# Performance work log

Hardware: AMD Instinct MI355X
Metric: run time of the kernel (lower is better)

Reference implementation:

```python
import jax, jax.numpy as jnp
import numpy as np

N_ENT = 50000
N_EDGE = 500000
D = 256          # ent_hidden_size
H1, C1 = 8, 64   # conv1: heads=8, out=64, concat -> 512
NEG_SLOPE = 0.2
LN_EPS = 1e-5


def setup_inputs() -> dict:
    key = jax.random.key(0)
    ks = jax.random.split(key, 12)
    s = 0.05  # small init scale for numerical sanity
    return {
        "edge_index": jax.random.randint(ks[0], (2, N_EDGE), 0, N_ENT),
        "x": jax.random.normal(ks[1], (N_ENT, D), dtype=jnp.float32),
        "ln_w": jnp.ones((D,), jnp.float32),
        "ln_b": jnp.zeros((D,), jnp.float32),
        "W1": jax.random.normal(ks[2], (D, H1 * C1), dtype=jnp.float32) * s,
        "att_src1": jax.random.normal(ks[3], (H1, C1), dtype=jnp.float32) * s,
        "att_dst1": jax.random.normal(ks[4], (H1, C1), dtype=jnp.float32) * s,
        "b1": jnp.zeros((H1 * C1,), jnp.float32),
        "W2": jax.random.normal(ks[5], (H1 * C1, D), dtype=jnp.float32) * s,
        "att_src2": jax.random.normal(ks[6], (1, D), dtype=jnp.float32) * s,
        "att_dst2": jax.random.normal(ks[7], (1, D), dtype=jnp.float32) * s,
        "b2": jnp.zeros((D,), jnp.float32),
    }


def _gat_conv(x, edge_index, W, att_src, att_dst, bias, heads, out_ch, concat):
    """PyG GATConv (shared src/dst lin, add_self_loops=True, eval-mode dropout)."""
    n = x.shape[0]
    loops = jnp.arange(n)
    src = jnp.concatenate([edge_index[0], loops])  # [E+N]
    dst = jnp.concatenate([edge_index[1], loops])

    h = (x @ W).reshape(n, heads, out_ch)                 # [N,H,C]
    a_src = jnp.sum(h * att_src[None], axis=-1)           # [N,H]
    a_dst = jnp.sum(h * att_dst[None], axis=-1)           # [N,H]

    e = jax.nn.leaky_relu(a_src[src] + a_dst[dst], NEG_SLOPE)  # [E+N,H]
    # per-destination segment softmax (every dst has a self-loop -> no empties)
    m = jax.lax.stop_gradient(jax.ops.segment_max(e, dst, num_segments=n))
    p = jnp.exp(e - m[dst])
    denom = jax.ops.segment_sum(p, dst, num_segments=n)
    alpha = p / denom[dst]                                # [E+N,H]

    out = jax.ops.segment_sum(h[src] * alpha[..., None], dst, num_segments=n)  # [N,H,C]
    out = out.reshape(n, heads * out_ch) if concat else out.mean(axis=1)
    return out + bias


def reference(edge_index, x, ln_w, ln_b, W1, att_src1, att_dst1, b1,
              W2, att_src2, att_dst2, b2):
    # LayerNorm(ent_hidden), eps=1e-5; dropouts are eval-mode no-ops
    mu = jnp.mean(x, axis=-1, keepdims=True)
    var = jnp.var(x, axis=-1, keepdims=True)
    h = (x - mu) / jnp.sqrt(var + LN_EPS) * ln_w + ln_b
    h = jax.nn.elu(_gat_conv(h, edge_index, W1, att_src1, att_dst1, b1, H1, C1, True))
    return _gat_conv(h, edge_index, W2, att_src2, att_dst2, b2, 1, D, False)
```

## Files before the change

### kernel.cpp

```cpp
#include <hip/hip_runtime.h>
#include <hip/hip_bf16.h>
#include <cstdint>

#define N_ENT  50000
#define N_EDGE 500000
#define D_IN   256
constexpr int ETOT = N_EDGE + N_ENT;

typedef __attribute__((ext_vector_type(8))) short bfrag;
typedef __attribute__((ext_vector_type(4))) float f4acc;
typedef __attribute__((ext_vector_type(4))) float f32x4;
typedef __attribute__((ext_vector_type(8))) short s16x8;

__device__ __forceinline__ float lrelu(float x) { return x > 0.f ? x : 0.2f * x; }
__device__ __forceinline__ float eluf(float x)  { return x > 0.f ? x : (expf(x) - 1.f); }
__device__ __forceinline__ short to_bf16(float f) {
    __hip_bfloat16 b = __float2bfloat16(f);
    return *(short*)&b;
}
__device__ __forceinline__ float2 bf2_to_f32(unsigned int u) {
    float2 r;
    r.x = __uint_as_float(u << 16);
    r.y = __uint_as_float(u & 0xffff0000u);
    return r;
}

__global__ __launch_bounds__(256) void prep_kernel(const float* __restrict__ x,
        const float* __restrict__ lnw, const float* __restrict__ lnb,
        short* __restrict__ y, const int* __restrict__ ei, int* __restrict__ cnt,
        const float* __restrict__ W1, short* __restrict__ W1T,
        const float* __restrict__ W2, short* __restrict__ W2T)
{
    int blk = blockIdx.x;
    if (blk < 12500) {
        int n = blk * 4 + (threadIdx.x >> 6);
        int lane = threadIdx.x & 63;
        const f32x4 v = __builtin_nontemporal_load((const f32x4*)(x + (size_t)n * D_IN + lane * 4));
        float s  = v.x + v.y + v.z + v.w;
        float sq = v.x*v.x + v.y*v.y + v.z*v.z + v.w*v.w;
        #pragma unroll
        for (int off = 1; off < 64; off <<= 1) {
            s  += __shfl_xor(s, off);
            sq += __shfl_xor(sq, off);
        }
        float mean = s * (1.f / 256.f);
        float var  = sq * (1.f / 256.f) - mean * mean;
        float rstd = rsqrtf(var + 1e-5f);
        float4 wv = *(const float4*)(lnw + lane * 4);
        float4 bv = *(const float4*)(lnb + lane * 4);
        short4 o;
        o.x = to_bf16((v.x - mean) * rstd * wv.x + bv.x);
        o.y = to_bf16((v.y - mean) * rstd * wv.y + bv.y);
        o.z = to_bf16((v.z - mean) * rstd * wv.z + bv.z);
        o.w = to_bf16((v.w - mean) * rstd * wv.w + bv.w);
        *(short4*)(y + (size_t)n * D_IN + lane * 4) = o;
    } else if (blk < 14454) {
        int e = (blk - 12500) * 256 + threadIdx.x;
        if (e < N_EDGE) atomicAdd(&cnt[ei[N_EDGE + e]], 1);
    } else if (blk < 14966) {
        int i = (blk - 14454) * 256 + threadIdx.x;
        int r = i >> 9, c = i & 511;
        W1T[c * 256 + r] = to_bf16(W1[i]);
    } else {
        int i = (blk - 14966) * 256 + threadIdx.x;
        int r = i >> 8, c = i & 255;
        W2T[c * 512 + r] = to_bf16(W2[i]);
    }
}

template<int NN, int KK, bool FUSE_DOTS>
__global__ __launch_bounds__(256) void gemm_mfma(const short* __restrict__ A,
        const short* __restrict__ BT, short* __restrict__ C,
        const float* __restrict__ att_s, const float* __restrict__ att_d,
        float* __restrict__ a_s, float* __restrict__ a_d, int M)
{
    __shared__ short As[128 * 32];
    __shared__ short Bs[128 * 32];
    const int tid  = threadIdx.x;
    const int w    = tid >> 6;
    const int l    = tid & 63;
    const int wm   = w >> 1, wn = w & 1;
    const int m0   = blockIdx.y * 128;
    const int n0   = blockIdx.x * 128;
    const int quad = l >> 4;
    const int ln16 = l & 15;
    const int rl   = l >> 2;
    const int cs   = l & 3;

    f4acc acc[4][4];
    #pragma unroll
    for (int i = 0; i < 4; ++i)
        #pragma unroll
        for (int j = 0; j < 4; ++j)
            acc[i][j] = (f4acc){0.f, 0.f, 0.f, 0.f};

    for (int k0 = 0; k0 < KK; k0 += 32) {
        __syncthreads();
        #pragma unroll
        for (int tt = 0; tt < 2; ++tt) {
            int t   = w * 2 + tt;
            int row = t * 16 + rl;
            int ca  = cs ^ ((row >> 1) & 3);
            const short* ga = A + (size_t)(m0 + row) * KK + k0 + ca * 8;
            __builtin_amdgcn_global_load_lds(
                (const __attribute__((address_space(1))) unsigned int*)ga,
                (__attribute__((address_space(3))) unsigned int*)&As[t * 512], 16, 0, 0);
            const short* gb = BT + (size_t)(n0 + row) * KK + k0 + ca * 8;
            __builtin_amdgcn_global_load_lds(
                (const __attribute__((address_space(1))) unsigned int*)gb,
                (__attribute__((address_space(3))) unsigned int*)&Bs[t * 512], 16, 0, 0);
        }
        __syncthreads();
        bfrag af[4], bf[4];
        #pragma unroll
        for (int i = 0; i < 4; ++i) {
            int r = wm * 64 + i * 16 + ln16;
            af[i] = *(const bfrag*)&As[r * 32 + (quad ^ ((r >> 1) & 3)) * 8];
            int rn = wn * 64 + i * 16 + ln16;
            bf[i] = *(const bfrag*)&Bs[rn * 32 + (quad ^ ((rn >> 1) & 3)) * 8];
        }
        #pragma unroll
        for (int i = 0; i < 4; ++i)
            #pragma unroll
            for (int j = 0; j < 4; ++j)
                acc[i][j] = __builtin_amdgcn_mfma_f32_16x16x32_bf16(af[i], bf[j], acc[i][j], 0, 0, 0);
    }

    float as_c[4], ad_c[4];
    if constexpr (FUSE_DOTS) {
        #pragma unroll
        for (int j = 0; j < 4; ++j) {
            int gc = n0 + wn * 64 + j * 16 + ln16;
            as_c[j] = att_s[gc];
            ad_c[j] = att_d[gc];
        }
    }
    const int hh = (n0 + wn * 64) >> 6;

    #pragma unroll
    for (int i = 0; i < 4; ++i) {
        #pragma unroll
        for (int p = 0; p < 4; ++p) {
            int gr = m0 + wm * 64 + i * 16 + quad * 4 + p;
            float ps = 0.f, pd = 0.f;
            if constexpr (FUSE_DOTS) {
                #pragma unroll
                for (int j = 0; j < 4; ++j) {
                    float c = acc[i][j][p];
                    ps = fmaf(c, as_c[j], ps);
                    pd = fmaf(c, ad_c[j], pd);
                }
                #pragma unroll
                for (int off = 1; off < 16; off <<= 1) {
                    ps += __shfl_xor(ps, off);
                    pd += __shfl_xor(pd, off);
                }
            }
            if (gr < M) {
                #pragma unroll
                for (int j = 0; j < 4; ++j) {
                    int gc = n0 + wn * 64 + j * 16 + ln16;
                    C[(size_t)gr * NN + gc] = to_bf16(acc[i][j][p]);
                }
                if constexpr (FUSE_DOTS) {
                    if (ln16 == 0) {
                        a_s[(size_t)gr * (NN / 64) + hh] = ps;
                        a_d[(size_t)gr * (NN / 64) + hh] = pd;
                    }
                }
            }
        }
    }
}

template<int H, int C>
__global__ __launch_bounds__(256) void attn_dots_kernel(const short* __restrict__ feat,
        const float* __restrict__ att_s, const float* __restrict__ att_d,
        float* __restrict__ a_s, float* __restrict__ a_d, int N)
{
    constexpr int F = H * C;
    constexpr int PL = F / 64;
    int n = blockIdx.x * 4 + (threadIdx.x >> 6);
    if (n >= N) return;
    int lane = threadIdx.x & 63;
    int f0 = lane * PL;
    int h = f0 / C;
    float fv[PL];
    const unsigned int* fp = (const unsigned int*)(feat + (size_t)n * F + f0);
    #pragma unroll
    for (int j = 0; j < PL / 2; ++j) {
        float2 t = bf2_to_f32(fp[j]);
        fv[2 * j] = t.x; fv[2 * j + 1] = t.y;
    }
    float ps = 0.f, pd = 0.f;
    #pragma unroll
    for (int j = 0; j < PL; ++j) {
        ps = fmaf(fv[j], att_s[f0 + j], ps);
        pd = fmaf(fv[j], att_d[f0 + j], pd);
    }
    constexpr int GROUP = 64 / H;
    #pragma unroll
    for (int off = 1; off < GROUP; off <<= 1) {
        ps += __shfl_xor(ps, off);
        pd += __shfl_xor(pd, off);
    }
    if ((lane & (GROUP - 1)) == 0) {
        a_s[(size_t)n * H + h] = ps;
        a_d[(size_t)n * H + h] = pd;
    }
}

__global__ __launch_bounds__(256) void alloc_kernel(const int* __restrict__ cnt,
        int* __restrict__ row_start, int* __restrict__ cursor)
{
    int d = blockIdx.x * 256 + threadIdx.x;
    int lane = threadIdx.x & 63;
    int c = (d < N_ENT) ? cnt[d] : 0;
    int inc = c;
    #pragma unroll
    for (int off = 1; off < 64; off <<= 1) {
        int nb = __shfl_up(inc, off);
        if (lane >= off) inc += nb;
    }
    int waveTotal = __shfl(inc, 63);
    int base = 0;
    if (lane == 63) base = atomicAdd(cursor, waveTotal);
    base = __shfl(base, 63);
    if (d < N_ENT) row_start[d] = base + inc - c;
}

__global__ __launch_bounds__(256) void fill_csr_kernel(const int* __restrict__ ei,
        const int* __restrict__ row_start, int* __restrict__ cursor2,
        int* __restrict__ csr_src)
{
    int e = blockIdx.x * 256 + threadIdx.x;
    if (e >= N_EDGE) return;
    int d = ei[N_EDGE + e];
    int pos = atomicAdd(&cursor2[d], 1);
    csr_src[row_start[d] + pos] = ei[e];
}

__global__ __launch_bounds__(256) void aggr1_kernel(const int* __restrict__ csr_src,
        const int* __restrict__ row_start, const int* __restrict__ cnt,
        const short* __restrict__ feat, const float* __restrict__ a_s,
        const float* __restrict__ a_d, const float* __restrict__ bias,
        short* __restrict__ out)
{
    int d = blockIdx.x * 4 + (threadIdx.x >> 6);
    if (d >= N_ENT) return;
    int lane = threadIdx.x & 63;
    int f0 = lane * 8;
    int h = lane >> 3;
    int rs = row_start[d];
    int n = cnt[d];
    float adh = a_d[d * 8 + h];

    float den = 0.f;
    float acc[8] = {0.f, 0.f, 0.f, 0.f, 0.f, 0.f, 0.f, 0.f};
    {
        float p = __expf(lrelu(a_s[d * 8 + h] + adh));
        den += p;
        uint4 rv = *(const uint4*)(feat + (size_t)d * 512 + f0);
        float2 t0 = bf2_to_f32(rv.x), t1 = bf2_to_f32(rv.y);
        float2 t2 = bf2_to_f32(rv.z), t3 = bf2_to_f32(rv.w);
        acc[0] += p * t0.x; acc[1] += p * t0.y; acc[2] += p * t1.x; acc[3] += p * t1.y;
        acc[4] += p * t2.x; acc[5] += p * t2.y; acc[6] += p * t3.x; acc[7] += p * t3.y;
    }
    int i = 0;
    for (; i + 4 <= n; i += 4) {
        int   sv[4];
        float ev[4];
        uint4 rv[4];
        #pragma unroll
        for (int u = 0; u < 4; ++u) sv[u] = csr_src[rs + i + u];
        #pragma unroll
        for (int u = 0; u < 4; ++u) ev[u] = a_s[sv[u] * 8 + h];
        #pragma unroll
        for (int u = 0; u < 4; ++u) rv[u] = *(const uint4*)(feat + (size_t)sv[u] * 512 + f0);
        #pragma unroll
        for (int u = 0; u < 4; ++u) {
            float p = __expf(lrelu(ev[u] + adh));
            den += p;
            float2 t0 = bf2_to_f32(rv[u].x), t1 = bf2_to_f32(rv[u].y);
            float2 t2 = bf2_to_f32(rv[u].z), t3 = bf2_to_f32(rv[u].w);
            acc[0] += p * t0.x; acc[1] += p * t0.y; acc[2] += p * t1.x; acc[3] += p * t1.y;
            acc[4] += p * t2.x; acc[5] += p * t2.y; acc[6] += p * t3.x; acc[7] += p * t3.y;
        }
    }
    for (; i < n; ++i) {
        int s = csr_src[rs + i];
        float p = __expf(lrelu(a_s[s * 8 + h] + adh));
        den += p;
        uint4 rv = *(const uint4*)(feat + (size_t)s * 512 + f0);
        float2 t0 = bf2_to_f32(rv.x), t1 = bf2_to_f32(rv.y);
        float2 t2 = bf2_to_f32(rv.z), t3 = bf2_to_f32(rv.w);
        acc[0] += p * t0.x; acc[1] += p * t0.y; acc[2] += p * t1.x; acc[3] += p * t1.y;
        acc[4] += p * t2.x; acc[5] += p * t2.y; acc[6] += p * t3.x; acc[7] += p * t3.y;
    }
    float inv = 1.f / den;
    float4 b0 = *(const float4*)(bias + f0);
    float4 b1 = *(const float4*)(bias + f0 + 4);
    s16x8 o;
    o[0] = to_bf16(eluf(acc[0] * inv + b0.x)); o[1] = to_bf16(eluf(acc[1] * inv + b0.y));
    o[2] = to_bf16(eluf(acc[2] * inv + b0.z)); o[3] = to_bf16(eluf(acc[3] * inv + b0.w));
    o[4] = to_bf16(eluf(acc[4] * inv + b1.x)); o[5] = to_bf16(eluf(acc[5] * inv + b1.y));
    o[6] = to_bf16(eluf(acc[6] * inv + b1.z)); o[7] = to_bf16(eluf(acc[7] * inv + b1.w));
    __builtin_nontemporal_store(o, (s16x8*)(out + (size_t)d * 512 + f0));
}

__global__ __launch_bounds__(256) void aggr2_kernel(const int* __restrict__ csr_src,
        const int* __restrict__ row_start, const int* __restrict__ cnt,
        const short* __restrict__ feat, const float* __restrict__ a_s,
        const float* __restrict__ a_d, const float* __restrict__ bias,
        float* __restrict__ out)
{
    int d = blockIdx.x * 4 + (threadIdx.x >> 6);
    if (d >= N_ENT) return;
    int lane = threadIdx.x & 63;
    int half = lane >> 5;
    int li   = lane & 31;
    int f0   = li * 8;
    int rs = row_start[d];
    int n = cnt[d];
    float adh = a_d[d];

    float den = 0.f;
    float acc[8] = {0.f, 0.f, 0.f, 0.f, 0.f, 0.f, 0.f, 0.f};
    {
        float p = (half == 0) ? __expf(lrelu(a_s[d] + adh)) : 0.f;
        uint4 rv = *(const uint4*)(feat + (size_t)d * 256 + f0);
        den += p;
        float2 t0 = bf2_to_f32(rv.x), t1 = bf2_to_f32(rv.y);
        float2 t2 = bf2_to_f32(rv.z), t3 = bf2_to_f32(rv.w);
        acc[0] += p * t0.x; acc[1] += p * t0.y; acc[2] += p * t1.x; acc[3] += p * t1.y;
        acc[4] += p * t2.x; acc[5] += p * t2.y; acc[6] += p * t3.x; acc[7] += p * t3.y;
    }
    int i = 0;
    for (; i + 4 <= n; i += 4) {
        int e0 = i + half, e1 = i + 2 + half;
        int s0 = csr_src[rs + e0];
        int s1 = csr_src[rs + e1];
        float a0 = a_s[s0], a1 = a_s[s1];
        uint4 rv0 = *(const uint4*)(feat + (size_t)s0 * 256 + f0);
        uint4 rv1 = *(const uint4*)(feat + (size_t)s1 * 256 + f0);
        float p0 = __expf(lrelu(a0 + adh));
        float p1 = __expf(lrelu(a1 + adh));
        den += p0 + p1;
        float2 t0, t1, t2, t3;
        t0 = bf2_to_f32(rv0.x); t1 = bf2_to_f32(rv0.y); t2 = bf2_to_f32(rv0.z); t3 = bf2_to_f32(rv0.w);
        acc[0] += p0 * t0.x; acc[1] += p0 * t0.y; acc[2] += p0 * t1.x; acc[3] += p0 * t1.y;
        acc[4] += p0 * t2.x; acc[5] += p0 * t2.y; acc[6] += p0 * t3.x; acc[7] += p0 * t3.y;
        t0 = bf2_to_f32(rv1.x); t1 = bf2_to_f32(rv1.y); t2 = bf2_to_f32(rv1.z); t3 = bf2_to_f32(rv1.w);
        acc[0] += p1 * t0.x; acc[1] += p1 * t0.y; acc[2] += p1 * t1.x; acc[3] += p1 * t1.y;
        acc[4] += p1 * t2.x; acc[5] += p1 * t2.y; acc[6] += p1 * t3.x; acc[7] += p1 * t3.y;
    }
    for (; i < n; i += 2) {
        int e = i + half;
        bool valid = e < n;
        int s = valid ? csr_src[rs + e] : d;
        float av = a_s[s];
        uint4 rv = *(const uint4*)(feat + (size_t)s * 256 + f0);
        float p = valid ? __expf(lrelu(av + adh)) : 0.f;
        den += p;
        float2 t0 = bf2_to_f32(rv.x), t1 = bf2_to_f32(rv.y);
        float2 t2 = bf2_to_f32(rv.z), t3 = bf2_to_f32(rv.w);
        acc[0] += p * t0.x; acc[1] += p * t0.y; acc[2] += p * t1.x; acc[3] += p * t1.y;
        acc[4] += p * t2.x; acc[5] += p * t2.y; acc[6] += p * t3.x; acc[7] += p * t3.y;
    }
    den += __shfl_xor(den, 32);
    #pragma unroll
    for (int k = 0; k < 8; ++k) acc[k] += __shfl_xor(acc[k], 32);

    float inv = 1.f / den;
    if (half == 0) {
        float4 b0 = *(const float4*)(bias + f0);
        float4 b1 = *(const float4*)(bias + f0 + 4);
        f32x4 o0, o1;
        o0.x = acc[0] * inv + b0.x; o0.y = acc[1] * inv + b0.y;
        o0.z = acc[2] * inv + b0.z; o0.w = acc[3] * inv + b0.w;
        o1.x = acc[4] * inv + b1.x; o1.y = acc[5] * inv + b1.y;
        o1.z = acc[6] * inv + b1.z; o1.w = acc[7] * inv + b1.w;
        __builtin_nontemporal_store(o0, (f32x4*)(out + (size_t)d * 256 + f0));
        __builtin_nontemporal_store(o1, (f32x4*)(out + (size_t)d * 256 + f0 + 4));
    }
}

extern "C" void kernel_launch(void* const* d_in, const int* in_sizes, int n_in,
                              void* d_out, int out_size, void* d_ws, size_t ws_size,
                              hipStream_t stream)
{
    const int*   ei     = (const int*)  d_in[0];
    const float* x      = (const float*)d_in[1];
    const float* ln_w   = (const float*)d_in[2];
    const float* ln_b   = (const float*)d_in[3];
    const float* W1     = (const float*)d_in[4];
    const float* att_s1 = (const float*)d_in[5];
    const float* att_d1 = (const float*)d_in[6];
    const float* b1     = (const float*)d_in[7];
    const float* W2     = (const float*)d_in[8];
    const float* att_s2 = (const float*)d_in[9];
    const float* att_d2 = (const float*)d_in[10];
    const float* b2     = (const float*)d_in[11];
    float* out = (float*)d_out;

    short* h0b = (short*)d_ws;
    short* h1b = h0b + 12800000;
    short* h2b = h1b + 25600000;
    short* h3b = h2b + 25600000;
    short* W1T = h3b + 12800000;
    short* W2T = W1T + 131072;
    float* a_s1 = (float*)(W2T + 131072);
    float* a_d1 = a_s1 + 400000;
    float* a_s2 = a_d1 + 400000;
    float* a_d2 = a_s2 + 50000;
    int* cnt       = (int*)(a_d2 + 50000);
    int* cursor2   = cnt + 50000;
    int* cursor    = cursor2 + 50000;
    int* row_start = cursor + 1;
    int* csr_src   = row_start + 50000;

    hipMemsetAsync(cnt, 0, 100001 * 4, stream);

    prep_kernel<<<15478, 256, 0, stream>>>(x, ln_w, ln_b, h0b, ei, cnt, W1, W1T, W2, W2T);
    alloc_kernel<<<196, 256, 0, stream>>>(cnt, row_start, cursor);
    fill_csr_kernel<<<1954, 256, 0, stream>>>(ei, row_start, cursor2, csr_src);

    gemm_mfma<512, 256, true><<<dim3(4, 391), 256, 0, stream>>>(
        h0b, W1T, h1b, att_s1, att_d1, a_s1, a_d1, N_ENT);
    aggr1_kernel<<<12500, 256, 0, stream>>>(csr_src, row_start, cnt, h1b, a_s1, a_d1, b1, h2b);

    gemm_mfma<256, 512, false><<<dim3(2, 391), 256, 0, stream>>>(
        h2b, W2T, h3b, nullptr, nullptr, nullptr, nullptr, N_ENT);
    attn_dots_kernel<1, 256><<<12500, 256, 0, stream>>>(h3b, att_s2, att_d2, a_s2, a_d2, N_ENT);
    aggr2_kernel<<<12500, 256, 0, stream>>>(csr_src, row_start, cnt, h3b, a_s2, a_d2, b2, out);
}
```

Measured before the change: 403.9 us.

## Fuse CSR fill into GEMM1 launch and attention dots into GEMM2 epilogue

Result: faster. 388.2 us (-3.9%).

```diff
diff --git a/kernel.cpp b/kernel.cpp
--- a/kernel.cpp
+++ b/kernel.cpp
@@ -68,20 +68,34 @@
     }
 }
 
-template<int NN, int KK, bool FUSE_DOTS>
+template<int NN, int KK, int CH, bool DO_FILL>
 __global__ __launch_bounds__(256) void gemm_mfma(const short* __restrict__ A,
         const short* __restrict__ BT, short* __restrict__ C,
         const float* __restrict__ att_s, const float* __restrict__ att_d,
-        float* __restrict__ a_s, float* __restrict__ a_d, int M)
-{
+        float* __restrict__ a_s, float* __restrict__ a_d, int M, int nGemm,
+        const int* __restrict__ ei, const int* __restrict__ row_start,
+        int* __restrict__ cursor2, int* __restrict__ csr_src)
+{
+    constexpr int GX = NN / 128;
     __shared__ short As[128 * 32];
     __shared__ short Bs[128 * 32];
+
+    if (DO_FILL && (int)blockIdx.x >= nGemm) {
+        int e = ((int)blockIdx.x - nGemm) * 256 + threadIdx.x;
+        if (e < N_EDGE) {
+            int d = ei[N_EDGE + e];
+            int pos = atomicAdd(&cursor2[d], 1);
+            csr_src[row_start[d] + pos] = ei[e];
+        }
+        return;
+    }
+
     const int tid  = threadIdx.x;
     const int w    = tid >> 6;
     const int l    = tid & 63;
     const int wm   = w >> 1, wn = w & 1;
-    const int m0   = blockIdx.y * 128;
-    const int n0   = blockIdx.x * 128;
+    const int m0   = ((int)blockIdx.x / GX) * 128;
+    const int n0   = ((int)blockIdx.x % GX) * 128;
     const int quad = l >> 4;
     const int ln16 = l & 15;
     const int rl   = l >> 2;
@@ -127,7 +141,7 @@
     }
 
     float as_c[4], ad_c[4];
-    if constexpr (FUSE_DOTS) {
+    if constexpr (CH > 0) {
         #pragma unroll
         for (int j = 0; j < 4; ++j) {
             int gc = n0 + wn * 64 + j * 16 + ln16;
@@ -143,7 +157,7 @@
         for (int p = 0; p < 4; ++p) {
             int gr = m0 + wm * 64 + i * 16 + quad * 4 + p;
             float ps = 0.f, pd = 0.f;
-            if constexpr (FUSE_DOTS) {
+            if constexpr (CH > 0) {
                 #pragma unroll
                 for (int j = 0; j < 4; ++j) {
                     float c = acc[i][j][p];
@@ -162,51 +176,19 @@
                     int gc = n0 + wn * 64 + j * 16 + ln16;
                     C[(size_t)gr * NN + gc] = to_bf16(acc[i][j][p]);
                 }
-                if constexpr (FUSE_DOTS) {
+                if constexpr (CH == 64) {
                     if (ln16 == 0) {
                         a_s[(size_t)gr * (NN / 64) + hh] = ps;
                         a_d[(size_t)gr * (NN / 64) + hh] = pd;
                     }
+                } else if constexpr (CH == 256) {
+                    if (ln16 == 0) {
+                        unsafeAtomicAdd(&a_s[gr], ps);
+                        unsafeAtomicAdd(&a_d[gr], pd);
+                    }
                 }
             }
         }
-    }
-}
-
-template<int H, int C>
-__global__ __launch_bounds__(256) void attn_dots_kernel(const short* __restrict__ feat,
-        const float* __restrict__ att_s, const float* __restrict__ att_d,
-        float* __restrict__ a_s, float* __restrict__ a_d, int N)
-{
-    constexpr int F = H * C;
-    constexpr int PL = F / 64;
-    int n = blockIdx.x * 4 + (threadIdx.x >> 6);
-    if (n >= N) return;
-    int lane = threadIdx.x & 63;
-    int f0 = lane * PL;
-    int h = f0 / C;
-    float fv[PL];
-    const unsigned int* fp = (const unsigned int*)(feat + (size_t)n * F + f0);
-    #pragma unroll
-    for (int j = 0; j < PL / 2; ++j) {
-        float2 t = bf2_to_f32(fp[j]);
-        fv[2 * j] = t.x; fv[2 * j + 1] = t.y;
-    }
-    float ps = 0.f, pd = 0.f;
-    #pragma unroll
-    for (int j = 0; j < PL; ++j) {
-        ps = fmaf(fv[j], att_s[f0 + j], ps);
-        pd = fmaf(fv[j], att_d[f0 + j], pd);
-    }
-    constexpr int GROUP = 64 / H;
-    #pragma unroll
-    for (int off = 1; off < GROUP; off <<= 1) {
-        ps += __shfl_xor(ps, off);
-        pd += __shfl_xor(pd, off);
-    }
-    if ((lane & (GROUP - 1)) == 0) {
-        a_s[(size_t)n * H + h] = ps;
-        a_d[(size_t)n * H + h] = pd;
     }
 }
 
@@ -227,17 +209,6 @@
     if (lane == 63) base = atomicAdd(cursor, waveTotal);
     base = __shfl(base, 63);
     if (d < N_ENT) row_start[d] = base + inc - c;
-}
-
-__global__ __launch_bounds__(256) void fill_csr_kernel(const int* __restrict__ ei,
-        const int* __restrict__ row_start, int* __restrict__ cursor2,
-        int* __restrict__ csr_src)
-{
-    int e = blockIdx.x * 256 + threadIdx.x;
-    if (e >= N_EDGE) return;
-    int d = ei[N_EDGE + e];
-    int pos = atomicAdd(&cursor2[d], 1);
-    csr_src[row_start[d] + pos] = ei[e];
 }
 
 __global__ __launch_bounds__(256) void aggr1_kernel(const int* __restrict__ csr_src,
@@ -419,18 +390,20 @@
     int* row_start = cursor + 1;
     int* csr_src   = row_start + 50000;
 
-    hipMemsetAsync(cnt, 0, 100001 * 4, stream);
+    hipMemsetAsync(a_s2, 0, 200001 * 4, stream);
 
     prep_kernel<<<15478, 256, 0, stream>>>(x, ln_w, ln_b, h0b, ei, cnt, W1, W1T, W2, W2T);
     alloc_kernel<<<196, 256, 0, stream>>>(cnt, row_start, cursor);
-    fill_csr_kernel<<<1954, 256, 0, stream>>>(ei, row_start, cursor2, csr_src);
-
-    gemm_mfma<512, 256, true><<<dim3(4, 391), 256, 0, stream>>>(
-        h0b, W1T, h1b, att_s1, att_d1, a_s1, a_d1, N_ENT);
+
+    constexpr int NG1 = 391 * 4;
+    gemm_mfma<512, 256, 64, true><<<NG1 + 1954, 256, 0, stream>>>(
+        h0b, W1T, h1b, att_s1, att_d1, a_s1, a_d1, N_ENT, NG1,
+        ei, row_start, cursor2, csr_src);
     aggr1_kernel<<<12500, 256, 0, stream>>>(csr_src, row_start, cnt, h1b, a_s1, a_d1, b1, h2b);
 
-    gemm_mfma<256, 512, false><<<dim3(2, 391), 256, 0, stream>>>(
-        h2b, W2T, h3b, nullptr, nullptr, nullptr, nullptr, N_ENT);
-    attn_dots_kernel<1, 256><<<12500, 256, 0, stream>>>(h3b, att_s2, att_d2, a_s2, a_d2, N_ENT);
+    constexpr int NG2 = 391 * 2;
+    gemm_mfma<256, 512, 256, false><<<NG2, 256, 0, stream>>>(
+        h2b, W2T, h3b, att_s2, att_d2, a_s2, a_d2, N_ENT, NG2,
+        nullptr, nullptr, nullptr, nullptr);
     aggr2_kernel<<<12500, 256, 0, stream>>>(csr_src, row_start, cnt, h3b, a_s2, a_d2, b2, out);
 }
```
